# Optimization experiments

Hardware: AMD Instinct MI355X
Metric: run time of the kernel (lower is better)

## Reference

```python
import jax, jax.numpy as jnp
import numpy as np

B, S, H, E = 32, 4096, 512, 512
NEG = -1000000000.0


def setup_inputs() -> dict:
    key = jax.random.key(0)
    ks = jax.random.split(key, 8)
    query = jax.random.normal(ks[0], (B, H), dtype=jnp.float32)
    keys = jax.random.normal(ks[1], (B, S, E), dtype=jnp.float32)
    mask = jax.random.randint(ks[2], (B, S), 0, 2, dtype=jnp.int32)
    # learned params (torch Linear: y = x @ W.T + b); store W already transposed
    Wq = jax.random.normal(ks[3], (H, H), dtype=jnp.float32) / np.sqrt(H)
    bq = jnp.zeros((H,), dtype=jnp.float32)
    Wk = jax.random.normal(ks[4], (E, H), dtype=jnp.float32) / np.sqrt(E)
    bk = jnp.zeros((H,), dtype=jnp.float32)
    v = jax.random.normal(ks[5], (H,), dtype=jnp.float32) / np.sqrt(H)
    bv = jnp.zeros((), dtype=jnp.float32)
    return {"query": query, "keys": keys, "mask": mask,
            "Wq": Wq, "bq": bq, "Wk": Wk, "bk": bk, "v": v, "bv": bv}


def reference(query, keys, mask, Wq, bq, Wk, bk, v, bv):
    # q_proj: (B, 1, H); k_proj: (B, S, H)
    q_proj = (query @ Wq + bq)[:, None, :]
    k_proj = jnp.einsum('bse,eh->bsh', keys, Wk) + bk
    # additive score: v^T tanh(q + k) + bv -> (B, S)
    scores = jnp.einsum('bsh,h->bs', jnp.tanh(q_proj + k_proj), v) + bv
    scores = jnp.where(mask == 0, NEG, scores)
    attn = jax.nn.softmax(scores, axis=-1)          # (B, S)
    context = jnp.einsum('bs,bse->be', attn, keys)  # (B, E)
    return context, attn
```

## Files before the change

### kernel.cpp

```cpp
#include <hip/hip_runtime.h>
#include <hip/hip_bf16.h>

#define BB 32
#define SS 4096
#define HH 512
#define EE 512
#define NCH 64
#define QSEG 8
#define NEGV -1000000000.0f

using float4v = __attribute__((ext_vector_type(4))) float;
using short8v = __attribute__((ext_vector_type(8))) short;

#if defined(__has_builtin)
#if __has_builtin(__builtin_amdgcn_sched_barrier)
#define SCHED_FENCE() __builtin_amdgcn_sched_barrier(0)
#endif
#if __has_builtin(__builtin_amdgcn_rcpf)
#define FAST_RCP(x) __builtin_amdgcn_rcpf(x)
#endif
#if __has_builtin(__builtin_amdgcn_exp2f)
#define FAST_EXP2(x) __builtin_amdgcn_exp2f(x)
#endif
#if __has_builtin(__builtin_amdgcn_s_setprio)
#define SETPRIO(n) __builtin_amdgcn_s_setprio(n)
#endif
#endif
#ifndef SCHED_FENCE
#define SCHED_FENCE()
#endif
#ifndef FAST_RCP
#define FAST_RCP(x) (1.0f / (x))
#endif
#ifndef FAST_EXP2
#define FAST_EXP2(x) __expf(0.69314718056f * (x))
#endif
#ifndef SETPRIO
#define SETPRIO(n)
#endif

__device__ inline unsigned short f2bf(float x) {
    union { float f; unsigned int u; } c; c.f = x;
    unsigned int r = c.u + 0x7FFFu + ((c.u >> 16) & 1u);
    return (unsigned short)(r >> 16);
}
__device__ inline float bf2f(unsigned short s) {
    union { float f; unsigned int u; } c; c.u = ((unsigned int)s) << 16;
    return c.f;
}
__device__ inline unsigned int pk2bf(float a, float b) {
    union { __hip_bfloat162 h; unsigned int u; } c;
    c.h = __float22bfloat162_rn(float2{a, b});
    return c.u;
}

__global__ void prep_kernel(const float* __restrict__ query, const float* __restrict__ Wq,
                            float* __restrict__ qp8,
                            const float* __restrict__ Wk, unsigned short* __restrict__ WkT) {
    int bx = blockIdx.x, t = threadIdx.x;
    if (bx < QSEG * BB) {
        __shared__ float qs[64];
        int b = bx >> 3, seg = bx & 7;
        if (t < 64) qs[t] = query[b * HH + seg * 64 + t];
        __syncthreads();
        float a0 = 0.f, a1 = 0.f;
        const float* wq = Wq + (size_t)(seg * 64) * HH;
        #pragma unroll 8
        for (int e = 0; e < 64; ++e) {
            float q = qs[e];
            a0 += q * wq[(size_t)e * HH + t];
            a1 += q * wq[(size_t)e * HH + t + 256];
        }
        qp8[((size_t)seg * BB + b) * HH + t] = a0;
        qp8[((size_t)seg * BB + b) * HH + t + 256] = a1;
    } else {
        int tile = bx - QSEG * BB;
        int ks = tile >> 3;
        int h0 = (tile & 7) * 64;
        __shared__ float wt[32][67];
        #pragma unroll
        for (int p = 0; p < 2; ++p) {
            int idx = t + p * 256;
            int r = idx >> 4, c4 = idx & 15;
            float4v wv = *(const float4v*)(Wk + (size_t)(ks * 32 + r) * HH + h0 + c4 * 4);
            wt[r][c4 * 4 + 0] = wv.x; wt[r][c4 * 4 + 1] = wv.y;
            wt[r][c4 * 4 + 2] = wv.z; wt[r][c4 * 4 + 3] = wv.w;
        }
        __syncthreads();
        int lane = t & 63, ntl = t >> 6;
        int lq = lane >> 4, lr = lane & 15;
        int nt = (h0 >> 4) + ntl;
        short8v o;
        #pragma unroll
        for (int j = 0; j < 8; ++j)
            o[j] = (short)f2bf(wt[lq * 8 + j][ntl * 16 + lr]);
        size_t g = ((size_t)ks * 32 + nt) * 64 + lane;
        *(short8v*)(WkT + g * 8) = o;
    }
}

__launch_bounds__(512, 2)
__global__ void fused_kernel(const float* __restrict__ keys, const unsigned short* __restrict__ WkT,
                             const float* __restrict__ qp8, const float* __restrict__ bq,
                             const float* __restrict__ bk, const float* __restrict__ v,
                             const float* __restrict__ bv, const int* __restrict__ mask,
                             float* __restrict__ pe_out, float* __restrict__ part,
                             float* __restrict__ marr, float* __restrict__ larr) {
    constexpr int LDK = EE + 8;
    __shared__ unsigned short klds[64 * LDK];
    __shared__ float qp_lds[HH];
    __shared__ float v_lds[HH];
    __shared__ float red[8][64];
    __shared__ float p_lds[64];
    __shared__ float ctxred[2][EE];
    int b = blockIdx.y, c = blockIdx.x, s0 = c * 64;
    int tid = threadIdx.x;

    const float4v* ksrc = (const float4v*)(keys + ((size_t)b * SS + s0) * EE);
    float4v kv[4];
    #pragma unroll
    for (int p = 0; p < 4; ++p) {
        int idx = tid + p * 512;
        kv[p] = ksrc[(size_t)(idx >> 5) * 128 + (idx & 31)];
    }
    int mval = 0;
    if (tid < 64) mval = mask[b * SS + s0 + tid];

    for (int i = tid; i < HH; i += 512) {
        float qv = 0.f;
        #pragma unroll
        for (int sg = 0; sg < QSEG; ++sg) qv += qp8[((size_t)sg * BB + b) * HH + i];
        qp_lds[i] = qv + bq[i] + bk[i];
        v_lds[i] = v[i];
    }

    #pragma unroll
    for (int p = 0; p < 4; ++p) {
        int idx = tid + p * 512, row = idx >> 5, c4 = idx & 31;
        unsigned int u0 = pk2bf(kv[p].x, kv[p].y), u1 = pk2bf(kv[p].z, kv[p].w);
        *(uint2*)(&klds[row * LDK + c4 * 4]) = make_uint2(u0, u1);
    }

    int w = tid >> 6, lane = tid & 63;
    int lq = lane >> 4, lr = lane & 15;
    int nt0 = w * 4;
    const short8v* Wf = (const short8v*)WkT;

    short8v bcur[4];
    #pragma unroll
    for (int j = 0; j < 4; ++j) bcur[j] = Wf[(size_t)(nt0 + j) * 64 + lane];

    float4v acc[4][4];
    #pragma unroll
    for (int m = 0; m < 4; ++m)
        #pragma unroll
        for (int j = 0; j < 4; ++j) acc[m][j] = (float4v){0.f, 0.f, 0.f, 0.f};

    __syncthreads();

    #pragma unroll
    for (int q = 0; q < 4; ++q) {
        if (q < 3) {
            #pragma unroll
            for (int p = 0; p < 4; ++p) {
                int idx = tid + p * 512;
                kv[p] = ksrc[(size_t)(idx >> 5) * 128 + (q + 1) * 32 + (idx & 31)];
            }
        }
        SCHED_FENCE();
        #pragma unroll
        for (int ksl = 0; ksl < 4; ++ksl) {
            int kq = q * 4 + ksl;
            short8v bn[4];
            if (kq < 15) {
                #pragma unroll
                for (int j = 0; j < 4; ++j)
                    bn[j] = Wf[((size_t)(kq + 1) * 32 + nt0 + j) * 64 + lane];
            }
            SETPRIO(1);
            #pragma unroll
            for (int m = 0; m < 4; ++m) {
                short8v afrag = *(const short8v*)(&klds[(m * 16 + lr) * LDK + kq * 32 + lq * 8]);
                #pragma unroll
                for (int j = 0; j < 4; ++j)
                    acc[m][j] = __builtin_amdgcn_mfma_f32_16x16x32_bf16(afrag, bcur[j], acc[m][j], 0, 0, 0);
            }
            SETPRIO(0);
            if (kq < 15) {
                #pragma unroll
                for (int j = 0; j < 4; ++j) bcur[j] = bn[j];
            }
            if (ksl == 2 && q < 3) {
                #pragma unroll
                for (int p = 0; p < 4; ++p) {
                    int idx = tid + p * 512, row = idx >> 5, c4 = (q + 1) * 32 + (idx & 31);
                    unsigned int u0 = pk2bf(kv[p].x, kv[p].y), u1 = pk2bf(kv[p].z, kv[p].w);
                    *(uint2*)(&klds[row * LDK + c4 * 4]) = make_uint2(u0, u1);
                }
            }
        }
        if (q < 3) __syncthreads();
    }

    float part_r[4][4];
    #pragma unroll
    for (int m = 0; m < 4; ++m)
        #pragma unroll
        for (int r = 0; r < 4; ++r) part_r[m][r] = 0.f;
    #pragma unroll
    for (int j = 0; j < 4; ++j) {
        int h = (nt0 + j) * 16 + lr;
        float vj = v_lds[h], qj = qp_lds[h], vj2 = -2.f * vj;
        #pragma unroll
        for (int m = 0; m < 4; ++m) {
            #pragma unroll
            for (int r = 0; r < 4; ++r) {
                float x = qj + acc[m][j][r];
                float rr = FAST_RCP(FAST_EXP2(2.885390082f * x) + 1.f);
                part_r[m][r] += __builtin_fmaf(vj2, rr, vj);
            }
        }
    }
    #pragma unroll
    for (int m = 0; m < 4; ++m)
        #pragma unroll
        for (int r = 0; r < 4; ++r) {
            float p = part_r[m][r];
            p += __shfl_xor(p, 1, 16);
            p += __shfl_xor(p, 2, 16);
            p += __shfl_xor(p, 4, 16);
            p += __shfl_xor(p, 8, 16);
            part_r[m][r] = p;
        }
    if (lr == 0) {
        #pragma unroll
        for (int m = 0; m < 4; ++m)
            #pragma unroll
            for (int r = 0; r < 4; ++r)
                red[w][m * 16 + lq * 4 + r] = part_r[m][r];
    }
    __syncthreads();

    if (tid < 64) {
        float sc = red[0][tid] + red[1][tid] + red[2][tid] + red[3][tid]
                 + red[4][tid] + red[5][tid] + red[6][tid] + red[7][tid] + bv[0];
        if (mval == 0) sc = NEGV;
        float mv = sc;
        #pragma unroll
        for (int off = 1; off < 64; off <<= 1) mv = fmaxf(mv, __shfl_xor(mv, off));
        float pe = __expf(sc - mv);
        float ls = pe;
        #pragma unroll
        for (int off = 1; off < 64; off <<= 1) ls += __shfl_xor(ls, off);
        p_lds[tid] = pe;
        pe_out[b * SS + s0 + tid] = pe;
        if (tid == 0) { marr[b * NCH + c] = mv; larr[b * NCH + c] = ls; }
    }
    __syncthreads();

    {
        int c2 = (tid & 255) * 2;
        int sb = (tid >> 8) * 32;
        float e0 = 0.f, e1 = 0.f;
        #pragma unroll 8
        for (int s = 0; s < 32; ++s) {
            unsigned int u = *(const unsigned int*)(&klds[(sb + s) * LDK + c2]);
            float ps = p_lds[sb + s];
            e0 = __builtin_fmaf(ps, bf2f((unsigned short)(u & 0xffffu)), e0);
            e1 = __builtin_fmaf(ps, bf2f((unsigned short)(u >> 16)), e1);
        }
        *(float2*)(&ctxred[tid >> 8][c2]) = make_float2(e0, e1);
    }
    __syncthreads();
    part[((size_t)b * NCH + c) * EE + tid] = ctxred[0][tid] + ctxred[1][tid];
}

__global__ void finalize_kernel(const float* __restrict__ pe_arr, const float* __restrict__ part,
                                const float* __restrict__ marr, const float* __restrict__ larr,
                                float* __restrict__ ctx, float* __restrict__ attn) {
    __shared__ float wgt[NCH];
    __shared__ float Ls;
    int b = blockIdx.y, px = blockIdx.x, t = threadIdx.x;
    if (t < NCH) {
        float m = marr[b * NCH + t], l = larr[b * NCH + t];
        float M = m;
        #pragma unroll
        for (int off = 1; off < 64; off <<= 1) M = fmaxf(M, __shfl_xor(M, off));
        float wq = __expf(m - M);
        float L = wq * l;
        #pragma unroll
        for (int off = 1; off < 64; off <<= 1) L += __shfl_xor(L, off);
        wgt[t] = wq;
        if (t == 0) Ls = L;
    }
    __syncthreads();
    float invL = 1.f / Ls;
    if (px == 0) {
        float o = 0.f;
        #pragma unroll 8
        for (int cc = 0; cc < NCH; ++cc)
            o += wgt[cc] * part[((size_t)b * NCH + cc) * EE + t];
        ctx[b * EE + t] = o * invL;
    }
    int s0 = px * 1024;
    attn[b * SS + s0 + t]       = pe_arr[b * SS + s0 + t]       * wgt[(s0 + t) >> 6]       * invL;
    attn[b * SS + s0 + t + 512] = pe_arr[b * SS + s0 + t + 512] * wgt[(s0 + t + 512) >> 6] * invL;
}

extern "C" void kernel_launch(void* const* d_in, const int* in_sizes, int n_in,
                              void* d_out, int out_size, void* d_ws, size_t ws_size,
                              hipStream_t stream) {
    const float* query = (const float*)d_in[0];
    const float* keys  = (const float*)d_in[1];
    const int*   mask  = (const int*)d_in[2];
    const float* Wq    = (const float*)d_in[3];
    const float* bq    = (const float*)d_in[4];
    const float* Wk    = (const float*)d_in[5];
    const float* bk    = (const float*)d_in[6];
    const float* v     = (const float*)d_in[7];
    const float* bv    = (const float*)d_in[8];

    float* out  = (float*)d_out;
    float* ctx  = out;
    float* attn = out + BB * EE;

    char* ws = (char*)d_ws;
    float* qp8          = (float*)ws;
    unsigned short* WkT = (unsigned short*)(ws + 524288);
    float* pe           = (float*)(ws + 1048576);
    float* part         = (float*)(ws + 1572864);
    float* marr         = (float*)(ws + 5767168);
    float* larr         = (float*)(ws + 5775360);

    prep_kernel<<<QSEG * BB + 128, 256, 0, stream>>>(query, Wq, qp8, Wk, WkT);
    fused_kernel<<<dim3(NCH, BB), 512, 0, stream>>>(keys, WkT, qp8, bq, bk, v, bv, mask,
                                                    pe, part, marr, larr);
    finalize_kernel<<<dim3(4, BB), 512, 0, stream>>>(pe, part, marr, larr, ctx, attn);
}
```

Before: 436.6 us.

## Double fused kernel block to 1024 threads with two-deep prefetch of keys and weights

The fused scoring kernel now runs 16 waves per block, each covering 2 of the 32 H-column tiles instead of 4. This halves per-thread accumulators and register use. Keys are prefetched two K-quarters ahead using two register sets, and Wk fragments are pipelined two k-steps deep. The bf16 LDS store for each next quarter moves to the end of the quarter, just before the barrier. The aim is more resident waves per CU to hide global-load latency, at the cost of more cross-wave reductions, larger shared buffers and tighter register limits from launch_bounds(1024,4).

Result: slower. 445.6 us (+2.1%).

```diff
diff --git a/kernel.cpp b/kernel.cpp
--- a/kernel.cpp
+++ b/kernel.cpp
@@ -99,7 +99,7 @@
     }
 }
 
-__launch_bounds__(512, 2)
+__launch_bounds__(1024, 4)
 __global__ void fused_kernel(const float* __restrict__ keys, const unsigned short* __restrict__ WkT,
                              const float* __restrict__ qp8, const float* __restrict__ bq,
                              const float* __restrict__ bk, const float* __restrict__ v,
@@ -110,23 +110,28 @@
     __shared__ unsigned short klds[64 * LDK];
     __shared__ float qp_lds[HH];
     __shared__ float v_lds[HH];
-    __shared__ float red[8][64];
+    __shared__ float red[16][64];
     __shared__ float p_lds[64];
-    __shared__ float ctxred[2][EE];
+    __shared__ float ctxred[4][EE];
     int b = blockIdx.y, c = blockIdx.x, s0 = c * 64;
     int tid = threadIdx.x;
 
     const float4v* ksrc = (const float4v*)(keys + ((size_t)b * SS + s0) * EE);
-    float4v kv[4];
-    #pragma unroll
-    for (int p = 0; p < 4; ++p) {
-        int idx = tid + p * 512;
-        kv[p] = ksrc[(size_t)(idx >> 5) * 128 + (idx & 31)];
+    float4v kva[2], kvb[2];
+    #pragma unroll
+    for (int p = 0; p < 2; ++p) {
+        int idx = tid + p * 1024;
+        kva[p] = ksrc[(size_t)(idx >> 5) * 128 + (idx & 31)];
+    }
+    #pragma unroll
+    for (int p = 0; p < 2; ++p) {
+        int idx = tid + p * 1024;
+        kvb[p] = ksrc[(size_t)(idx >> 5) * 128 + 32 + (idx & 31)];
     }
     int mval = 0;
     if (tid < 64) mval = mask[b * SS + s0 + tid];
 
-    for (int i = tid; i < HH; i += 512) {
+    for (int i = tid; i < HH; i += 1024) {
         float qv = 0.f;
         #pragma unroll
         for (int sg = 0; sg < QSEG; ++sg) qv += qp8[((size_t)sg * BB + b) * HH + i];
@@ -135,81 +140,82 @@
     }
 
     #pragma unroll
-    for (int p = 0; p < 4; ++p) {
-        int idx = tid + p * 512, row = idx >> 5, c4 = idx & 31;
-        unsigned int u0 = pk2bf(kv[p].x, kv[p].y), u1 = pk2bf(kv[p].z, kv[p].w);
+    for (int p = 0; p < 2; ++p) {
+        int idx = tid + p * 1024, row = idx >> 5, c4 = idx & 31;
+        unsigned int u0 = pk2bf(kva[p].x, kva[p].y), u1 = pk2bf(kva[p].z, kva[p].w);
         *(uint2*)(&klds[row * LDK + c4 * 4]) = make_uint2(u0, u1);
     }
 
     int w = tid >> 6, lane = tid & 63;
     int lq = lane >> 4, lr = lane & 15;
-    int nt0 = w * 4;
+    int nt_lo = w * 2;
     const short8v* Wf = (const short8v*)WkT;
 
-    short8v bcur[4];
-    #pragma unroll
-    for (int j = 0; j < 4; ++j) bcur[j] = Wf[(size_t)(nt0 + j) * 64 + lane];
-
-    float4v acc[4][4];
+    short8v bf0[2], bf1[2], bf2[2];
+    #pragma unroll
+    for (int j = 0; j < 2; ++j) bf0[j] = Wf[(size_t)(nt_lo + j) * 64 + lane];
+    #pragma unroll
+    for (int j = 0; j < 2; ++j) bf1[j] = Wf[((size_t)32 + nt_lo + j) * 64 + lane];
+
+    float4v acc[4][2];
     #pragma unroll
     for (int m = 0; m < 4; ++m)
         #pragma unroll
-        for (int j = 0; j < 4; ++j) acc[m][j] = (float4v){0.f, 0.f, 0.f, 0.f};
+        for (int j = 0; j < 2; ++j) acc[m][j] = (float4v){0.f, 0.f, 0.f, 0.f};
 
     __syncthreads();
 
     #pragma unroll
     for (int q = 0; q < 4; ++q) {
-        if (q < 3) {
-            #pragma unroll
-            for (int p = 0; p < 4; ++p) {
-                int idx = tid + p * 512;
-                kv[p] = ksrc[(size_t)(idx >> 5) * 128 + (q + 1) * 32 + (idx & 31)];
+        if (q < 2) {
+            #pragma unroll
+            for (int p = 0; p < 2; ++p) {
+                int idx = tid + p * 1024;
+                float4v t4 = ksrc[(size_t)(idx >> 5) * 128 + (q + 2) * 32 + (idx & 31)];
+                if (q == 0) kva[p] = t4; else kvb[p] = t4;
             }
         }
         SCHED_FENCE();
         #pragma unroll
         for (int ksl = 0; ksl < 4; ++ksl) {
             int kq = q * 4 + ksl;
-            short8v bn[4];
-            if (kq < 15) {
+            if (kq < 14) {
                 #pragma unroll
-                for (int j = 0; j < 4; ++j)
-                    bn[j] = Wf[((size_t)(kq + 1) * 32 + nt0 + j) * 64 + lane];
+                for (int j = 0; j < 2; ++j)
+                    bf2[j] = Wf[((size_t)(kq + 2) * 32 + nt_lo + j) * 64 + lane];
             }
             SETPRIO(1);
             #pragma unroll
             for (int m = 0; m < 4; ++m) {
                 short8v afrag = *(const short8v*)(&klds[(m * 16 + lr) * LDK + kq * 32 + lq * 8]);
                 #pragma unroll
-                for (int j = 0; j < 4; ++j)
-                    acc[m][j] = __builtin_amdgcn_mfma_f32_16x16x32_bf16(afrag, bcur[j], acc[m][j], 0, 0, 0);
+                for (int j = 0; j < 2; ++j)
+                    acc[m][j] = __builtin_amdgcn_mfma_f32_16x16x32_bf16(afrag, bf0[j], acc[m][j], 0, 0, 0);
             }
             SETPRIO(0);
-            if (kq < 15) {
-                #pragma unroll
-                for (int j = 0; j < 4; ++j) bcur[j] = bn[j];
-            }
-            if (ksl == 2 && q < 3) {
-                #pragma unroll
-                for (int p = 0; p < 4; ++p) {
-                    int idx = tid + p * 512, row = idx >> 5, c4 = (q + 1) * 32 + (idx & 31);
-                    unsigned int u0 = pk2bf(kv[p].x, kv[p].y), u1 = pk2bf(kv[p].z, kv[p].w);
-                    *(uint2*)(&klds[row * LDK + c4 * 4]) = make_uint2(u0, u1);
-                }
-            }
-        }
-        if (q < 3) __syncthreads();
-    }
-
-    float part_r[4][4];
+            #pragma unroll
+            for (int j = 0; j < 2; ++j) { bf0[j] = bf1[j]; bf1[j] = bf2[j]; }
+        }
+        if (q < 3) {
+            #pragma unroll
+            for (int p = 0; p < 2; ++p) {
+                int idx = tid + p * 1024, row = idx >> 5, c4 = (q + 1) * 32 + (idx & 31);
+                float4v t4 = (q & 1) ? kva[p] : kvb[p];
+                unsigned int u0 = pk2bf(t4.x, t4.y), u1 = pk2bf(t4.z, t4.w);
+                *(uint2*)(&klds[row * LDK + c4 * 4]) = make_uint2(u0, u1);
+            }
+            __syncthreads();
+        }
+    }
+
+    float pr[4][4];
     #pragma unroll
     for (int m = 0; m < 4; ++m)
         #pragma unroll
-        for (int r = 0; r < 4; ++r) part_r[m][r] = 0.f;
-    #pragma unroll
-    for (int j = 0; j < 4; ++j) {
-        int h = (nt0 + j) * 16 + lr;
+        for (int r = 0; r < 4; ++r) pr[m][r] = 0.f;
+    #pragma unroll
+    for (int j = 0; j < 2; ++j) {
+        int h = (nt_lo + j) * 16 + lr;
         float vj = v_lds[h], qj = qp_lds[h], vj2 = -2.f * vj;
         #pragma unroll
         for (int m = 0; m < 4; ++m) {
@@ -217,7 +223,7 @@
             for (int r = 0; r < 4; ++r) {
                 float x = qj + acc[m][j][r];
                 float rr = FAST_RCP(FAST_EXP2(2.885390082f * x) + 1.f);
-                part_r[m][r] += __builtin_fmaf(vj2, rr, vj);
+                pr[m][r] += __builtin_fmaf(vj2, rr, vj);
             }
         }
     }
@@ -225,25 +231,26 @@
     for (int m = 0; m < 4; ++m)
         #pragma unroll
         for (int r = 0; r < 4; ++r) {
-            float p = part_r[m][r];
+            float p = pr[m][r];
             p += __shfl_xor(p, 1, 16);
             p += __shfl_xor(p, 2, 16);
             p += __shfl_xor(p, 4, 16);
             p += __shfl_xor(p, 8, 16);
-            part_r[m][r] = p;
+            pr[m][r] = p;
         }
     if (lr == 0) {
         #pragma unroll
         for (int m = 0; m < 4; ++m)
             #pragma unroll
             for (int r = 0; r < 4; ++r)
-                red[w][m * 16 + lq * 4 + r] = part_r[m][r];
+                red[w][m * 16 + lq * 4 + r] = pr[m][r];
     }
     __syncthreads();
 
     if (tid < 64) {
-        float sc = red[0][tid] + red[1][tid] + red[2][tid] + red[3][tid]
-                 + red[4][tid] + red[5][tid] + red[6][tid] + red[7][tid] + bv[0];
+        float sc = bv[0];
+        #pragma unroll
+        for (int ww = 0; ww < 16; ++ww) sc += red[ww][tid];
         if (mval == 0) sc = NEGV;
         float mv = sc;
         #pragma unroll
@@ -259,20 +266,22 @@
     __syncthreads();
 
     {
-        int c2 = (tid & 255) * 2;
-        int sb = (tid >> 8) * 32;
+        int rq = tid >> 8, c2 = (tid & 255) * 2;
         float e0 = 0.f, e1 = 0.f;
         #pragma unroll 8
-        for (int s = 0; s < 32; ++s) {
-            unsigned int u = *(const unsigned int*)(&klds[(sb + s) * LDK + c2]);
-            float ps = p_lds[sb + s];
+        for (int s = 0; s < 16; ++s) {
+            int row = rq * 16 + s;
+            unsigned int u = *(const unsigned int*)(&klds[row * LDK + c2]);
+            float ps = p_lds[row];
             e0 = __builtin_fmaf(ps, bf2f((unsigned short)(u & 0xffffu)), e0);
             e1 = __builtin_fmaf(ps, bf2f((unsigned short)(u >> 16)), e1);
         }
-        *(float2*)(&ctxred[tid >> 8][c2]) = make_float2(e0, e1);
-    }
-    __syncthreads();
-    part[((size_t)b * NCH + c) * EE + tid] = ctxred[0][tid] + ctxred[1][tid];
+        *(float2*)(&ctxred[rq][c2]) = make_float2(e0, e1);
+    }
+    __syncthreads();
+    if (tid < EE)
+        part[((size_t)b * NCH + c) * EE + tid] =
+            ctxred[0][tid] + ctxred[1][tid] + ctxred[2][tid] + ctxred[3][tid];
 }
 
 __global__ void finalize_kernel(const float* __restrict__ pe_arr, const float* __restrict__ part,
@@ -333,7 +342,7 @@
     float* larr         = (float*)(ws + 5775360);
 
     prep_kernel<<<QSEG * BB + 128, 256, 0, stream>>>(query, Wq, qp8, Wk, WkT);
-    fused_kernel<<<dim3(NCH, BB), 512, 0, stream>>>(keys, WkT, qp8, bq, bk, v, bv, mask,
-                                                    pe, part, marr, larr);
+    fused_kernel<<<dim3(NCH, BB), 1024, 0, stream>>>(keys, WkT, qp8, bq, bk, v, bv, mask,
+                                                     pe, part, marr, larr);
     finalize_kernel<<<dim3(4, BB), 512, 0, stream>>>(pe, part, marr, larr, ctx, attn);
 }
```
